# Kernel optimization log

Hardware: AMD Instinct MI355X
Metric: run time of the kernel (lower is better)

The kernel has to match this reference:

```python
import jax, jax.numpy as jnp
import numpy as np

S, B, D, H = 2048, 2, 1024, 16
DK = D // H


def _rope_tables(seq_len, dk):
    inv_freq = 1.0 / (10000.0 ** (np.arange(0, dk, 2, dtype=np.float32) / dk))
    ang = np.arange(seq_len, dtype=np.float32)[:, None] * inv_freq[None, :]  # [S, dk/2]
    ang = np.concatenate([ang, ang], axis=-1)  # [S, dk]
    cos = jnp.asarray(np.cos(ang))[None, None]  # [1,1,S,dk]
    sin = jnp.asarray(np.sin(ang))[None, None]
    return cos, sin


def rotate_half(x):
    x1, x2 = x[..., : x.shape[-1] // 2], x[..., x.shape[-1] // 2 :]
    return jnp.concatenate([-x2, x1], axis=-1)


def apply_rope(x, cos, sin):
    return x * cos + rotate_half(x) * sin


def setup_inputs() -> dict:
    key = jax.random.key(0)
    ks = jax.random.split(key, 12)
    Q = jax.random.normal(ks[0], (S, B, D), dtype=jnp.float32)
    K = jax.random.normal(ks[1], (S, B, D), dtype=jnp.float32)
    V = jax.random.normal(ks[2], (S, B, D), dtype=jnp.float32)
    s = 0.02
    W_q = jax.random.normal(ks[3], (D, D), dtype=jnp.float32) * s
    W_k = jax.random.normal(ks[4], (D, D), dtype=jnp.float32) * s
    W_v = jax.random.normal(ks[5], (D, D), dtype=jnp.float32) * s
    W_o = jax.random.normal(ks[6], (D, D), dtype=jnp.float32) * s
    b_q = jnp.zeros((D,), jnp.float32)
    b_k = jnp.zeros((D,), jnp.float32)
    b_v = jnp.zeros((D,), jnp.float32)
    b_o = jnp.zeros((D,), jnp.float32)
    cos, sin = _rope_tables(S, DK)
    mask = jnp.triu(jnp.ones((S, S), dtype=bool), k=1)[None, None]  # causal, True = masked
    return {
        "Q": Q, "K": K, "V": V,
        "W_q": W_q, "b_q": b_q, "W_k": W_k, "b_k": b_k,
        "W_v": W_v, "b_v": b_v, "W_o": W_o, "b_o": b_o,
        "q_rotary_cos": cos, "q_rotary_sin": sin,
        "k_rotary_cos": cos, "k_rotary_sin": sin,
        "mask": mask,
    }


def reference(Q, K, V, W_q, b_q, W_k, b_k, W_v, b_v, W_o, b_o,
              q_rotary_cos, q_rotary_sin, k_rotary_cos, k_rotary_sin, mask):
    q_len, bsz, _ = Q.shape
    # [S,B,D] -> [S,B,H,dk] -> [B,H,S,dk]
    def proj(x, W, b):
        y = x @ W.T + b
        return y.reshape(x.shape[0], bsz, H, DK).transpose(1, 2, 0, 3)
    q_s = apply_rope(proj(Q, W_q, b_q), q_rotary_cos, q_rotary_sin)
    k_s = apply_rope(proj(K, W_k, b_k), k_rotary_cos, k_rotary_sin)
    v_s = proj(V, W_v, b_v)
    scores = jnp.einsum("bhqd,bhkd->bhqk", q_s, k_s) / jnp.sqrt(jnp.float32(DK))
    scores = jnp.where(mask, jnp.float32(-1e9), scores)
    attn = jax.nn.softmax(scores, axis=-1)
    context = jnp.einsum("bhqk,bhkd->bhqd", attn, v_s)  # [B,H,S,dk]
    context = context.transpose(2, 0, 1, 3).reshape(q_len, bsz, D)
    return context @ W_o.T + b_o
```

## Files before the change

### kernel.cpp

```cpp
#include <hip/hip_runtime.h>
#include <cstdint>
#include <cstddef>

typedef __bf16 bf16;
typedef __bf16 bf16x2 __attribute__((ext_vector_type(2)));
typedef __bf16 bf16x4 __attribute__((ext_vector_type(4)));
typedef __bf16 bf16x8 __attribute__((ext_vector_type(8)));
typedef float f32x4 __attribute__((ext_vector_type(4)));

#define S_LEN 2048
#define BATCH 2
#define DM 1024
#define NH 16
#define DKH 64
#define MTOT (S_LEN * BATCH)

__device__ __forceinline__ void gload_lds16(const void* g, void* l) {
    __builtin_amdgcn_global_load_lds((const __attribute__((address_space(1))) uint32_t*)g,
                                     (__attribute__((address_space(3))) uint32_t*)l, 16, 0, 0);
}

__device__ __forceinline__ uint32_t pack2(float a, float b) {
    bf16x2 v; v[0] = (bf16)a; v[1] = (bf16)b;
    return __builtin_bit_cast(uint32_t, v);
}

struct ConvArgs { const float* src[7]; bf16* dst[7]; };

__global__ __launch_bounds__(256) void convert_all(ConvArgs a) {
    int gid = blockIdx.x * 256 + threadIdx.x;
    int tid, off;
    if (gid < 3 * 524288) { tid = gid >> 19; off = gid & 524287; }
    else { int r = gid - 3 * 524288; tid = 3 + (r >> 17); off = r & 131071; }
    const float4* s4 = (const float4*)a.src[tid];
    float4 x = s4[2 * off], y = s4[2 * off + 1];
    bf16x8 v;
    v[0] = (bf16)x.x; v[1] = (bf16)x.y; v[2] = (bf16)x.z; v[3] = (bf16)x.w;
    v[4] = (bf16)y.x; v[5] = (bf16)y.y; v[6] = (bf16)y.z; v[7] = (bf16)y.w;
    *(bf16x8*)(a.dst[tid] + 8 * (size_t)off) = v;
}

__device__ __forceinline__ void gemm_core(const bf16* __restrict__ A, const bf16* __restrict__ Bt,
                                          const float* __restrict__ bias, void* __restrict__ out,
                                          int mode, const float* __restrict__ cosp,
                                          const float* __restrict__ sinp, bf16* As, bf16* Bs) {
    const int K = DM;
    int t = threadIdx.x;
    int lane = t & 63, wave = t >> 6;
    int lm = lane & 15, quad = lane >> 4;
    int m0 = blockIdx.y * 128, n0 = blockIdx.x * 128;
    int wm = (wave >> 1) * 64, wn = (wave & 1) * 64;
    f32x4 acc[4][4] = {};
    int g0 = t, g1 = t + 256;
    const bf16* agp0 = A + (size_t)(m0 + (g0 >> 2)) * K + (g0 & 3) * 8;
    const bf16* agp1 = A + (size_t)(m0 + (g1 >> 2)) * K + (g1 & 3) * 8;
    const bf16* bgp0 = Bt + (size_t)(n0 + (g0 >> 2)) * K + (g0 & 3) * 8;
    const bf16* bgp1 = Bt + (size_t)(n0 + (g1 >> 2)) * K + (g1 & 3) * 8;
    bf16* al0 = As + wave * 512;
    bf16* al1 = As + 2048 + wave * 512;
    bf16* bl0 = Bs + wave * 512;
    bf16* bl1 = Bs + 2048 + wave * 512;
    for (int k0 = 0; k0 < K; k0 += 32) {
        gload_lds16(agp0 + k0, al0);
        gload_lds16(agp1 + k0, al1);
        gload_lds16(bgp0 + k0, bl0);
        gload_lds16(bgp1 + k0, bl1);
        __syncthreads();
        bf16x8 af[4], bfr[4];
#pragma unroll
        for (int i = 0; i < 4; ++i)
            af[i] = *(const bf16x8*)(As + (wm + i * 16 + lm) * 32 + quad * 8);
#pragma unroll
        for (int j = 0; j < 4; ++j)
            bfr[j] = *(const bf16x8*)(Bs + (wn + j * 16 + lm) * 32 + quad * 8);
        if (mode == 1) {
#pragma unroll
            for (int i = 0; i < 4; ++i)
#pragma unroll
                for (int j = 0; j < 4; ++j)
                    acc[i][j] = __builtin_amdgcn_mfma_f32_16x16x32_bf16(bfr[j], af[i], acc[i][j], 0, 0, 0);
        } else {
#pragma unroll
            for (int i = 0; i < 4; ++i)
#pragma unroll
                for (int j = 0; j < 4; ++j)
                    acc[i][j] = __builtin_amdgcn_mfma_f32_16x16x32_bf16(af[i], bfr[j], acc[i][j], 0, 0, 0);
        }
        __syncthreads();
    }
    if (mode == 1) {
#pragma unroll
        for (int j = 0; j < 4; ++j) {
#pragma unroll
            for (int r = 0; r < 4; ++r) {
                int d = n0 + wn + j * 16 + quad * 4 + r;
                float bv = bias[d];
                int h = d >> 6, dk = d & 63;
#pragma unroll
                for (int i = 0; i < 4; ++i) {
                    int token = m0 + wm + i * 16 + lm;
                    int s = token >> 1, b = token & 1;
                    ((bf16*)out)[((size_t)(b * NH + h) * DKH + dk) * S_LEN + s] =
                        (bf16)(acc[i][j][r] + bv);
                }
            }
        }
        return;
    }
#pragma unroll
    for (int j = 0; j < 4; ++j) {
        float bcol = bias[n0 + wn + j * 16 + lm];
#pragma unroll
        for (int i = 0; i < 4; ++i)
#pragma unroll
            for (int r = 0; r < 4; ++r) acc[i][j][r] += bcol;
    }
#pragma unroll
    for (int i = 0; i < 4; ++i) {
#pragma unroll
        for (int j = 0; j < 4; ++j) {
            int col = n0 + wn + j * 16 + lm;
#pragma unroll
            for (int r = 0; r < 4; ++r) {
                int row = m0 + wm + i * 16 + quad * 4 + r;
                float val = acc[i][j][r];
                if (mode == 2) {
                    ((float*)out)[(size_t)row * DM + col] = val;
                } else {
                    int s = row >> 1, dk = col & 63;
                    float c = cosp[s * 64 + dk], sn = sinp[s * 64 + dk];
                    float partner = acc[i][j ^ 2][r];
                    float v2 = val * c + (dk < 32 ? -partner : partner) * sn;
                    if (mode == 3) v2 *= 0.125f * 1.44269504088896f;
                    ((bf16*)out)[(size_t)row * DM + col] = (bf16)v2;
                }
            }
        }
    }
}

struct QKVArgs {
    const bf16* A[3]; const bf16* W[3]; const float* bias[3];
    void* out[3]; const float* cs[3]; const float* sn[3]; int mode[3];
};

__global__ __launch_bounds__(256) void gemm_qkv(QKVArgs args) {
    __shared__ __align__(16) bf16 As[128 * 32];
    __shared__ __align__(16) bf16 Bs[128 * 32];
    int z = blockIdx.z;
    gemm_core(args.A[z], args.W[z], args.bias[z], args.out[z], args.mode[z],
              args.cs[z], args.sn[z], As, Bs);
}

__global__ __launch_bounds__(256) void gemm_one(const bf16* __restrict__ A, const bf16* __restrict__ Bt,
                                                const float* __restrict__ bias, void* __restrict__ out) {
    __shared__ __align__(16) bf16 As[128 * 32];
    __shared__ __align__(16) bf16 Bs[128 * 32];
    gemm_core(A, Bt, bias, out, 2, nullptr, nullptr, As, Bs);
}

__global__ __launch_bounds__(256, 2) void flash_kernel(const bf16* __restrict__ qp, const bf16* __restrict__ kp,
                                                       const bf16* __restrict__ vT, bf16* __restrict__ ctx) {
    int qta = blockIdx.x;
    int qtb = 31 - qta;
    int bh = blockIdx.y;
    int b = bh >> 4, h = bh & 15;
    int t = threadIdx.x, lane = t & 63, wave = t >> 6;
    int lm = lane & 15, quad = lane >> 4;
    __shared__ __align__(16) bf16 Ks[64 * 64];
    __shared__ __align__(16) bf16 Vs[64 * 64];
    __shared__ __align__(16) uint32_t Pb[4][16 * 37];
    uint32_t* pw = &Pb[wave][0];
    const int q0[2] = {qta * 64 + wave * 16, qtb * 64 + wave * 16};

    bf16x8 aq[2][2];
#pragma unroll
    for (int u = 0; u < 2; ++u) {
        const bf16* qrow = qp + ((size_t)(q0[u] + lm) * BATCH + b) * DM + h * DKH;
        aq[u][0] = *(const bf16x8*)(qrow + quad * 8);
        aq[u][1] = *(const bf16x8*)(qrow + 32 + quad * 8);
    }
    f32x4 o[2][4] = {};
    float l_acc[2] = {0.f, 0.f};

    int r0 = t >> 3, c0 = t & 7;
    int r1 = r0 + 32;
    const bf16* kg0 = kp + ((size_t)r0 * BATCH + b) * DM + h * DKH + c0 * 8;
    const bf16* kg1 = kp + ((size_t)r1 * BATCH + b) * DM + h * DKH + c0 * 8;
    const bf16* vg0 = vT + ((size_t)(bh * DKH + r0)) * S_LEN + c0 * 8;
    const bf16* vg1 = vT + ((size_t)(bh * DKH + r1)) * S_LEN + c0 * 8;
    int lk0 = r0 * 64 + (c0 ^ (r0 & 7)) * 8;
    int lk1 = r1 * 64 + (c0 ^ (r1 & 7)) * 8;
    const size_t kstep = (size_t)64 * BATCH * DM;

    const int niter = qtb + 1;
    bf16x8 ka = *(const bf16x8*)kg0;
    bf16x8 kb2 = *(const bf16x8*)kg1;
    bf16x8 va = *(const bf16x8*)vg0;
    bf16x8 vb2 = *(const bf16x8*)vg1;
    *(bf16x8*)(Ks + lk0) = ka;
    *(bf16x8*)(Ks + lk1) = kb2;
    *(bf16x8*)(Vs + lk0) = va;
    *(bf16x8*)(Vs + lk1) = vb2;
    __syncthreads();

    for (int it = 0; it < niter; ++it) {
        int kv0 = it << 6;
        bool hn = (it + 1) < niter;
        if (hn) {
            size_t koff = (size_t)(it + 1) * kstep;
            ka  = *(const bf16x8*)(kg0 + koff);
            kb2 = *(const bf16x8*)(kg1 + koff);
            va  = *(const bf16x8*)(vg0 + (it + 1) * 64);
            vb2 = *(const bf16x8*)(vg1 + (it + 1) * 64);
        }
        bf16x8 kf[4][2];
#pragma unroll
        for (int nt = 0; nt < 4; ++nt) {
            int krow = nt * 16 + lm;
            kf[nt][0] = *(const bf16x8*)(Ks + krow * 64 + ((quad ^ (krow & 7)) * 8));
            kf[nt][1] = *(const bf16x8*)(Ks + krow * 64 + (((quad + 4) ^ (krow & 7)) * 8));
        }
#pragma unroll
        for (int u = 0; u < 2; ++u) {
            if (u == 0 && kv0 > q0[0] + 15) continue;
            const f32x4 zero = {0.f, 0.f, 0.f, 0.f};
            f32x4 sc[4];
#pragma unroll
            for (int nt = 0; nt < 4; ++nt) {
                sc[nt] = __builtin_amdgcn_mfma_f32_16x16x32_bf16(kf[nt][0], aq[u][0], zero, 0, 0, 0);
                sc[nt] = __builtin_amdgcn_mfma_f32_16x16x32_bf16(kf[nt][1], aq[u][1], sc[nt], 0, 0, 0);
            }
            if (kv0 + 63 > q0[u]) {
#pragma unroll
                for (int nt = 0; nt < 4; ++nt)
#pragma unroll
                    for (int r = 0; r < 4; ++r) {
                        int kvg = kv0 + nt * 16 + quad * 4 + r;
                        if (kvg > q0[u] + lm) sc[nt][r] = -1e30f;
                    }
            }
            float rs = 0.f;
            uint32_t pk[8];
#pragma unroll
            for (int nt = 0; nt < 4; ++nt)
#pragma unroll
                for (int rp = 0; rp < 2; ++rp) {
                    float p0 = exp2f(sc[nt][2 * rp]);
                    float p1 = exp2f(sc[nt][2 * rp + 1]);
                    rs += p0 + p1;
                    pk[nt * 2 + rp] = pack2(p0, p1);
                }
            l_acc[u] += rs;
#pragma unroll
            for (int nt = 0; nt < 4; ++nt)
#pragma unroll
                for (int rp = 0; rp < 2; ++rp)
                    pw[lm * 37 + nt * 8 + quad * 2 + rp] = pk[nt * 2 + rp];
            __builtin_amdgcn_wave_barrier();
            const uint32_t* pr = pw + lm * 37;
            bf16x8 pf0 = *(const bf16x8*)(pr + quad * 4);
            bf16x8 pf1 = *(const bf16x8*)(pr + 16 + quad * 4);
#pragma unroll
            for (int dt = 0; dt < 4; ++dt) {
                int vrow = dt * 16 + lm;
                bf16x8 vf0 = *(const bf16x8*)(Vs + vrow * 64 + ((quad ^ (vrow & 7)) * 8));
                bf16x8 vf1 = *(const bf16x8*)(Vs + vrow * 64 + (((quad + 4) ^ (vrow & 7)) * 8));
                o[u][dt] = __builtin_amdgcn_mfma_f32_16x16x32_bf16(vf0, pf0, o[u][dt], 0, 0, 0);
                o[u][dt] = __builtin_amdgcn_mfma_f32_16x16x32_bf16(vf1, pf1, o[u][dt], 0, 0, 0);
            }
            __builtin_amdgcn_wave_barrier();
        }
        __syncthreads();
        if (hn) {
            *(bf16x8*)(Ks + lk0) = ka;
            *(bf16x8*)(Ks + lk1) = kb2;
            *(bf16x8*)(Vs + lk0) = va;
            *(bf16x8*)(Vs + lk1) = vb2;
        }
        __syncthreads();
    }
#pragma unroll
    for (int u = 0; u < 2; ++u) {
        float l = l_acc[u];
        l += __shfl_xor(l, 16, 64);
        l += __shfl_xor(l, 32, 64);
        float linv = 1.f / l;
        int qg = q0[u] + lm;
        bf16* crow = ctx + ((size_t)qg * BATCH + b) * DM + h * DKH;
#pragma unroll
        for (int dt = 0; dt < 4; ++dt) {
            bf16x4 v;
#pragma unroll
            for (int r = 0; r < 4; ++r) v[r] = (bf16)(o[u][dt][r] * linv);
            *(bf16x4*)(crow + dt * 16 + quad * 4) = v;
        }
    }
}

extern "C" void kernel_launch(void* const* d_in, const int* in_sizes, int n_in,
                              void* d_out, int out_size, void* d_ws, size_t ws_size,
                              hipStream_t stream) {
    const float* Q    = (const float*)d_in[0];
    const float* K    = (const float*)d_in[1];
    const float* V    = (const float*)d_in[2];
    const float* Wq   = (const float*)d_in[3];
    const float* bq   = (const float*)d_in[4];
    const float* Wk   = (const float*)d_in[5];
    const float* bk   = (const float*)d_in[6];
    const float* Wv   = (const float*)d_in[7];
    const float* bv   = (const float*)d_in[8];
    const float* Wo   = (const float*)d_in[9];
    const float* bo   = (const float*)d_in[10];
    const float* qcos = (const float*)d_in[11];
    const float* qsin = (const float*)d_in[12];
    const float* kcos = (const float*)d_in[13];
    const float* ksin = (const float*)d_in[14];

    char* ws = (char*)d_ws;
    const size_t SZ_ACT = (size_t)MTOT * DM * sizeof(bf16);
    const size_t SZ_W   = (size_t)DM * DM * sizeof(bf16);
    bf16* qb  = (bf16*)ws; ws += SZ_ACT;
    bf16* kb  = (bf16*)ws; ws += SZ_ACT;
    bf16* vb  = (bf16*)ws; ws += SZ_ACT;
    bf16* wqb = (bf16*)ws; ws += SZ_W;
    bf16* wkb = (bf16*)ws; ws += SZ_W;
    bf16* wvb = (bf16*)ws; ws += SZ_W;
    bf16* wob = (bf16*)ws; ws += SZ_W;
    bf16* qpr = (bf16*)ws; ws += SZ_ACT;
    bf16* kpr = (bf16*)ws; ws += SZ_ACT;
    bf16* vTp = (bf16*)ws; ws += SZ_ACT;
    bf16* ctx = (bf16*)ws; ws += SZ_ACT;

    ConvArgs ca;
    ca.src[0] = Q;  ca.dst[0] = qb;
    ca.src[1] = K;  ca.dst[1] = kb;
    ca.src[2] = V;  ca.dst[2] = vb;
    ca.src[3] = Wq; ca.dst[3] = wqb;
    ca.src[4] = Wk; ca.dst[4] = wkb;
    ca.src[5] = Wv; ca.dst[5] = wvb;
    ca.src[6] = Wo; ca.dst[6] = wob;
    convert_all<<<8192, 256, 0, stream>>>(ca);

    QKVArgs qa;
    qa.A[0] = qb; qa.W[0] = wqb; qa.bias[0] = bq; qa.out[0] = qpr; qa.mode[0] = 3; qa.cs[0] = qcos; qa.sn[0] = qsin;
    qa.A[1] = kb; qa.W[1] = wkb; qa.bias[1] = bk; qa.out[1] = kpr; qa.mode[1] = 4; qa.cs[1] = kcos; qa.sn[1] = ksin;
    qa.A[2] = vb; qa.W[2] = wvb; qa.bias[2] = bv; qa.out[2] = vTp; qa.mode[2] = 1; qa.cs[2] = nullptr; qa.sn[2] = nullptr;
    gemm_qkv<<<dim3(DM / 128, MTOT / 128, 3), 256, 0, stream>>>(qa);

    flash_kernel<<<dim3(16, BATCH * NH), 256, 0, stream>>>(qpr, kpr, vTp, ctx);

    gemm_one<<<dim3(DM / 128, MTOT / 128), 256, 0, stream>>>(ctx, wob, bo, (float*)d_out);
}
```

Baseline: 285.8 us.

## Switch projection GEMMs to single-wave 64x64 tiles without block barriers

The QKV and output projection GEMMs now run one wave per block on a 64x64 output tile instead of four waves on 128x128. The block-wide __syncthreads pair becomes a vmcnt wait plus wave barriers, so no cross-wave synchronisation is needed. The grid gets four times more, smaller blocks with M on the x dimension, which can raise occupancy and cut barrier stalls. In exchange each loaded A/B row is reused across fewer outputs, so global and LDS traffic per FLOP doubles, and the load-then-compute loop has no double buffering.

Result: faster. 279.5 us (-2.2%).

```diff
diff --git a/kernel.cpp b/kernel.cpp
--- a/kernel.cpp
+++ b/kernel.cpp
@@ -46,33 +46,27 @@
                                           const float* __restrict__ sinp, bf16* As, bf16* Bs) {
     const int K = DM;
     int t = threadIdx.x;
-    int lane = t & 63, wave = t >> 6;
-    int lm = lane & 15, quad = lane >> 4;
-    int m0 = blockIdx.y * 128, n0 = blockIdx.x * 128;
-    int wm = (wave >> 1) * 64, wn = (wave & 1) * 64;
+    int lm = t & 15, quad = t >> 4;
+    int m0 = blockIdx.x * 64, n0 = blockIdx.y * 64;
     f32x4 acc[4][4] = {};
-    int g0 = t, g1 = t + 256;
-    const bf16* agp0 = A + (size_t)(m0 + (g0 >> 2)) * K + (g0 & 3) * 8;
-    const bf16* agp1 = A + (size_t)(m0 + (g1 >> 2)) * K + (g1 & 3) * 8;
-    const bf16* bgp0 = Bt + (size_t)(n0 + (g0 >> 2)) * K + (g0 & 3) * 8;
-    const bf16* bgp1 = Bt + (size_t)(n0 + (g1 >> 2)) * K + (g1 & 3) * 8;
-    bf16* al0 = As + wave * 512;
-    bf16* al1 = As + 2048 + wave * 512;
-    bf16* bl0 = Bs + wave * 512;
-    bf16* bl1 = Bs + 2048 + wave * 512;
+    const bf16* agp = A + (size_t)(m0 + (t >> 2)) * K + (t & 3) * 8;
+    const bf16* bgp = Bt + (size_t)(n0 + (t >> 2)) * K + (t & 3) * 8;
+
     for (int k0 = 0; k0 < K; k0 += 32) {
-        gload_lds16(agp0 + k0, al0);
-        gload_lds16(agp1 + k0, al1);
-        gload_lds16(bgp0 + k0, bl0);
-        gload_lds16(bgp1 + k0, bl1);
-        __syncthreads();
+#pragma unroll
+        for (int i = 0; i < 4; ++i) {
+            gload_lds16(agp + (size_t)i * 16 * K + k0, As + i * 512);
+            gload_lds16(bgp + (size_t)i * 16 * K + k0, Bs + i * 512);
+        }
+        __builtin_amdgcn_s_waitcnt(0x0070);
+        __builtin_amdgcn_wave_barrier();
         bf16x8 af[4], bfr[4];
 #pragma unroll
         for (int i = 0; i < 4; ++i)
-            af[i] = *(const bf16x8*)(As + (wm + i * 16 + lm) * 32 + quad * 8);
+            af[i] = *(const bf16x8*)(As + (i * 16 + lm) * 32 + quad * 8);
 #pragma unroll
         for (int j = 0; j < 4; ++j)
-            bfr[j] = *(const bf16x8*)(Bs + (wn + j * 16 + lm) * 32 + quad * 8);
+            bfr[j] = *(const bf16x8*)(Bs + (j * 16 + lm) * 32 + quad * 8);
         if (mode == 1) {
 #pragma unroll
             for (int i = 0; i < 4; ++i)
@@ -86,19 +80,19 @@
                 for (int j = 0; j < 4; ++j)
                     acc[i][j] = __builtin_amdgcn_mfma_f32_16x16x32_bf16(af[i], bfr[j], acc[i][j], 0, 0, 0);
         }
-        __syncthreads();
+        __builtin_amdgcn_wave_barrier();
     }
     if (mode == 1) {
 #pragma unroll
         for (int j = 0; j < 4; ++j) {
 #pragma unroll
             for (int r = 0; r < 4; ++r) {
-                int d = n0 + wn + j * 16 + quad * 4 + r;
+                int d = n0 + j * 16 + quad * 4 + r;
                 float bv = bias[d];
                 int h = d >> 6, dk = d & 63;
 #pragma unroll
                 for (int i = 0; i < 4; ++i) {
-                    int token = m0 + wm + i * 16 + lm;
+                    int token = m0 + i * 16 + lm;
                     int s = token >> 1, b = token & 1;
                     ((bf16*)out)[((size_t)(b * NH + h) * DKH + dk) * S_LEN + s] =
                         (bf16)(acc[i][j][r] + bv);
@@ -109,7 +103,7 @@
     }
 #pragma unroll
     for (int j = 0; j < 4; ++j) {
-        float bcol = bias[n0 + wn + j * 16 + lm];
+        float bcol = bias[n0 + j * 16 + lm];
 #pragma unroll
         for (int i = 0; i < 4; ++i)
 #pragma unroll
@@ -119,10 +113,10 @@
     for (int i = 0; i < 4; ++i) {
 #pragma unroll
         for (int j = 0; j < 4; ++j) {
-            int col = n0 + wn + j * 16 + lm;
+            int col = n0 + j * 16 + lm;
 #pragma unroll
             for (int r = 0; r < 4; ++r) {
-                int row = m0 + wm + i * 16 + quad * 4 + r;
+                int row = m0 + i * 16 + quad * 4 + r;
                 float val = acc[i][j][r];
                 if (mode == 2) {
                     ((float*)out)[(size_t)row * DM + col] = val;
@@ -144,18 +138,18 @@
     void* out[3]; const float* cs[3]; const float* sn[3]; int mode[3];
 };
 
-__global__ __launch_bounds__(256) void gemm_qkv(QKVArgs args) {
-    __shared__ __align__(16) bf16 As[128 * 32];
-    __shared__ __align__(16) bf16 Bs[128 * 32];
+__global__ __launch_bounds__(64) void gemm_qkv(QKVArgs args) {
+    __shared__ __align__(16) bf16 As[64 * 32];
+    __shared__ __align__(16) bf16 Bs[64 * 32];
     int z = blockIdx.z;
     gemm_core(args.A[z], args.W[z], args.bias[z], args.out[z], args.mode[z],
               args.cs[z], args.sn[z], As, Bs);
 }
 
-__global__ __launch_bounds__(256) void gemm_one(const bf16* __restrict__ A, const bf16* __restrict__ Bt,
-                                                const float* __restrict__ bias, void* __restrict__ out) {
-    __shared__ __align__(16) bf16 As[128 * 32];
-    __shared__ __align__(16) bf16 Bs[128 * 32];
+__global__ __launch_bounds__(64) void gemm_one(const bf16* __restrict__ A, const bf16* __restrict__ Bt,
+                                               const float* __restrict__ bias, void* __restrict__ out) {
+    __shared__ __align__(16) bf16 As[64 * 32];
+    __shared__ __align__(16) bf16 Bs[64 * 32];
     gemm_core(A, Bt, bias, out, 2, nullptr, nullptr, As, Bs);
 }
 
@@ -346,9 +340,9 @@
     qa.A[0] = qb; qa.W[0] = wqb; qa.bias[0] = bq; qa.out[0] = qpr; qa.mode[0] = 3; qa.cs[0] = qcos; qa.sn[0] = qsin;
     qa.A[1] = kb; qa.W[1] = wkb; qa.bias[1] = bk; qa.out[1] = kpr; qa.mode[1] = 4; qa.cs[1] = kcos; qa.sn[1] = ksin;
     qa.A[2] = vb; qa.W[2] = wvb; qa.bias[2] = bv; qa.out[2] = vTp; qa.mode[2] = 1; qa.cs[2] = nullptr; qa.sn[2] = nullptr;
-    gemm_qkv<<<dim3(DM / 128, MTOT / 128, 3), 256, 0, stream>>>(qa);
+    gemm_qkv<<<dim3(MTOT / 64, DM / 64, 3), 64, 0, stream>>>(qa);
 
     flash_kernel<<<dim3(16, BATCH * NH), 256, 0, stream>>>(qpr, kpr, vTp, ctx);
 
-    gemm_one<<<dim3(DM / 128, MTOT / 128), 256, 0, stream>>>(ctx, wob, bo, (float*)d_out);
-}
+    gemm_one<<<dim3(MTOT / 64, DM / 64), 64, 0, stream>>>(ctx, wob, bo, (float*)d_out);
+}
```
